# Kernel tuning notes

Hardware: AMD Instinct MI355X
Metric: run time of the kernel (lower is better)

Reference implementation:

```python
import jax, jax.numpy as jnp
import numpy as np

NUM_HEADS = 8
D_MODEL = 512
D_K = D_MODEL // NUM_HEADS


def setup_inputs() -> dict:
    key = jax.random.key(0)
    ks = jax.random.split(key, 8)
    B, C, L = 4, D_MODEL, 2048
    s = 1.0 / np.sqrt(C)  # xavier-ish scale for 1x1 convs
    return {
        "X_q": jax.random.normal(ks[0], (B, C, L), jnp.float32),
        "X_k": jax.random.normal(ks[1], (B, C, L), jnp.float32),
        "X_v": jax.random.normal(ks[2], (B, C, L), jnp.float32),
        "Wq": jax.random.normal(ks[3], (D_MODEL, C), jnp.float32) * s,
        "Wk": jax.random.normal(ks[4], (D_MODEL, C), jnp.float32) * s,
        "Wv": jax.random.normal(ks[5], (D_MODEL, C), jnp.float32) * s,
        "Wh": jax.random.normal(ks[6], (D_MODEL, D_MODEL), jnp.float32) * s,
        "bh": jnp.zeros((D_MODEL,), jnp.float32),
    }


def reference(X_q, X_k, X_v, Wq, Wk, Wv, Wh, bh):
    B, C, L = X_q.shape
    H, dk = NUM_HEADS, D_K

    def proj(x, W):  # 1x1 Conv1d, no bias: (B,Cin,L) -> (B,Cout,L)
        return jnp.einsum("oc,bcl->bol", W, x)

    # split_heads: (B, d_model, L) -> (B, H, d_k, L)
    Q = proj(X_q, Wq).reshape(B, H, dk, L)
    K = proj(X_k, Wk).reshape(B, H, dk, L)
    V = proj(X_v, Wv).reshape(B, H, dk, L)

    Q = Q / np.sqrt(dk).astype(np.float32)
    # scores: Q^T K -> (B, H, L_q, L_k)
    scores = jnp.einsum("bhdq,bhdk->bhqk", Q, K)
    A = jax.nn.softmax(scores, axis=-1)
    # H = A @ V^T -> (B, H, L, d_k); dropout is identity at eval
    Hh = jnp.einsum("bhqk,bhdk->bhqd", A, V)
    # group_heads: (B,H,L,dk) -> (B,H,dk,L) -> (B, d_model, L)
    H_cat = Hh.transpose(0, 1, 3, 2).reshape(B, H * dk, L)
    out = jnp.einsum("oc,bcl->bol", Wh, H_cat) + bh[None, :, None]
    return (out, A)
```

## Files before the change

### kernel.cpp

```cpp
#include <hip/hip_runtime.h>

#define L_SEQ 2048
#define CDIM  512
#define NB    4
#define NH    8
#define DKH   64

typedef __attribute__((ext_vector_type(8))) __bf16 bf16x8;
typedef __attribute__((ext_vector_type(4))) float  f32x4;
typedef __attribute__((ext_vector_type(8))) unsigned short u16x8;

__device__ __forceinline__ unsigned short f2bf(float f) {
  union { float f; unsigned u; } x; x.f = f;
  unsigned r = x.u + 0x7FFFu + ((x.u >> 16) & 1u);
  return (unsigned short)(r >> 16);
}
__device__ __forceinline__ float bf2f(unsigned short u) {
  union { unsigned u; float f; } x; x.u = ((unsigned)u) << 16;
  return x.f;
}
__device__ __forceinline__ bf16x8 ldfrag(const unsigned short* p) {
  u16x8 v = *reinterpret_cast<const u16x8*>(p);
  return __builtin_bit_cast(bf16x8, v);
}
#define MFMA(a,b,c) __builtin_amdgcn_mfma_f32_16x16x32_bf16((a),(b),(c),0,0,0)

__global__ __launch_bounds__(256) void k_cast(const float* __restrict__ X,
                                              unsigned short* __restrict__ Y, int n) {
  int i = (blockIdx.x * 256 + threadIdx.x) * 8;
  if (i + 8 > n) return;
  const float4* p = reinterpret_cast<const float4*>(X + i);
  float4 a = p[0], b = p[1];
  u16x8 o;
  o[0]=f2bf(a.x); o[1]=f2bf(a.y); o[2]=f2bf(a.z); o[3]=f2bf(a.w);
  o[4]=f2bf(b.x); o[5]=f2bf(b.y); o[6]=f2bf(b.z); o[7]=f2bf(b.w);
  *reinterpret_cast<u16x8*>(Y + i) = o;
}

__global__ __launch_bounds__(256) void k_transpose(const float* __restrict__ X,
                                                   unsigned short* __restrict__ Xt) {
  __shared__ __align__(16) unsigned short t[64][72];
  int l0 = blockIdx.x * 64, c0 = blockIdx.y * 64;
  size_t boff = (size_t)blockIdx.z * CDIM * L_SEQ;
  const float* Xb = X + boff;
  unsigned short* Xtb = Xt + boff;
  int tid = threadIdx.x;
  int cc = tid >> 2, lo = (tid & 3) * 16;
  const float* src = Xb + (size_t)(c0 + cc) * L_SEQ + l0 + lo;
#pragma unroll
  for (int i = 0; i < 4; ++i) {
    float4 v = *reinterpret_cast<const float4*>(src + i * 4);
    t[lo + i*4 + 0][cc] = f2bf(v.x);
    t[lo + i*4 + 1][cc] = f2bf(v.y);
    t[lo + i*4 + 2][cc] = f2bf(v.z);
    t[lo + i*4 + 3][cc] = f2bf(v.w);
  }
  __syncthreads();
  int ll = tid >> 2, co = (tid & 3) * 16;
  unsigned short* dst = Xtb + (size_t)(l0 + ll) * CDIM + c0 + co;
  u16x8 a = *reinterpret_cast<const u16x8*>(&t[ll][co]);
  u16x8 b = *reinterpret_cast<const u16x8*>(&t[ll][co + 8]);
  *reinterpret_cast<u16x8*>(dst) = a;
  *reinterpret_cast<u16x8*>(dst + 8) = b;
}

template<int OUT_BF16, int HAS_BIAS>
__global__ __launch_bounds__(256) void k_gemm_nt(
    const unsigned short* __restrict__ A, long sA,
    const unsigned short* __restrict__ Bt, long sB,
    void* __restrict__ Out, long sO,
    const float* __restrict__ bias, float scale, int M, int N) {
  __shared__ __align__(16) unsigned short lA[128 * 64];
  __shared__ __align__(16) unsigned short lB[128 * 64];
  int b = blockIdx.z;
  const unsigned short* Ab = A + (size_t)b * sA;
  const unsigned short* Bb = Bt + (size_t)b * sB;
  int m0 = blockIdx.y * 128, n0 = blockIdx.x * 128;
  int tid = threadIdx.x, lane = tid & 63, wave = tid >> 6;
  int wm = (wave >> 1) * 64, wn = (wave & 1) * 64;
  f32x4 acc[4][4] = {};
  int srow = tid >> 3;
  int sslot = tid & 7;

  for (int k0 = 0; k0 < 512; k0 += 64) {
    __syncthreads();
#pragma unroll
    for (int i = 0; i < 4; ++i) {
      int r = srow + 32 * i;
      int sw = (sslot ^ (r & 7)) * 8;
      u16x8 va = *reinterpret_cast<const u16x8*>(Ab + (size_t)(m0 + r) * 512 + k0 + sslot * 8);
      *reinterpret_cast<u16x8*>(&lA[r * 64 + sw]) = va;
      u16x8 vb = *reinterpret_cast<const u16x8*>(Bb + (size_t)(n0 + r) * 512 + k0 + sslot * 8);
      *reinterpret_cast<u16x8*>(&lB[r * 64 + sw]) = vb;
    }
    __syncthreads();
#pragma unroll
    for (int c = 0; c < 2; ++c) {
      bf16x8 af[4], bfr[4];
#pragma unroll
      for (int t = 0; t < 4; ++t) {
        int ra = wm + t * 16 + (lane & 15);
        int sa = (lane >> 4) + 4 * c;
        af[t] = ldfrag(&lA[ra * 64 + ((sa ^ (ra & 7)) * 8)]);
        int rb = wn + t * 16 + (lane & 15);
        bfr[t] = ldfrag(&lB[rb * 64 + ((sa ^ (rb & 7)) * 8)]);
      }
#pragma unroll
      for (int i = 0; i < 4; ++i)
#pragma unroll
        for (int j = 0; j < 4; ++j)
          acc[i][j] = MFMA(af[i], bfr[j], acc[i][j]);
    }
  }
  int row4 = (lane >> 4) * 4, col = lane & 15;
#pragma unroll
  for (int i = 0; i < 4; ++i)
#pragma unroll
    for (int j = 0; j < 4; ++j)
#pragma unroll
      for (int e = 0; e < 4; ++e) {
        int r = m0 + wm + i * 16 + row4 + e;
        int cN = n0 + wn + j * 16 + col;
        float v = acc[i][j][e] * scale;
        if (HAS_BIAS) v += bias[r];
        size_t idx = (size_t)b * sO + (size_t)r * N + cN;
        if (OUT_BF16) ((unsigned short*)Out)[idx] = f2bf(v);
        else          ((float*)Out)[idx] = v;
      }
}

__global__ __launch_bounds__(256) void k_attn(
    const unsigned short* __restrict__ Qt,
    const unsigned short* __restrict__ Kt,
    const unsigned short* __restrict__ Vn,
    unsigned short* __restrict__ HhT,
    float* __restrict__ Aout) {
  __shared__ __align__(16) unsigned short a_lds[4][1024];
  int bh = blockIdx.y;
  int b = bh >> 3, h = bh & 7;
  int lane = threadIdx.x & 63, wave = threadIdx.x >> 6;
  int q0 = blockIdx.x * 64 + wave * 16;
  const unsigned short* Qh = Qt + (size_t)b * L_SEQ * CDIM + h * DKH;
  const unsigned short* Kh = Kt + (size_t)b * L_SEQ * CDIM + h * DKH;
  const unsigned short* Vh = Vn + (size_t)b * CDIM * L_SEQ + (size_t)h * DKH * L_SEQ;
  unsigned short* Ho = HhT + (size_t)b * L_SEQ * CDIM + h * DKH;
  float* Ab = Aout + (size_t)bh * L_SEQ * L_SEQ;

  int fr = lane & 15, fg = lane >> 4;
  bf16x8 qf0 = ldfrag(Qh + (size_t)(q0 + fr) * CDIM + fg * 8);
  bf16x8 qf1 = ldfrag(Qh + (size_t)(q0 + fr) * CDIM + fg * 8 + 32);

  float psum[4] = {0.f, 0.f, 0.f, 0.f};
  for (int kt = 0; kt < L_SEQ; kt += 64) {
#pragma unroll
    for (int t = 0; t < 4; ++t) {
      const unsigned short* kp = Kh + (size_t)(kt + t * 16 + fr) * CDIM + fg * 8;
      f32x4 s = {0.f, 0.f, 0.f, 0.f};
      s = MFMA(qf0, ldfrag(kp), s);
      s = MFMA(qf1, ldfrag(kp + 32), s);
#pragma unroll
      for (int e = 0; e < 4; ++e) psum[e] += __expf(s[e]);
    }
  }
#pragma unroll
  for (int e = 0; e < 4; ++e) {
    psum[e] += __shfl_xor(psum[e], 1, 64);
    psum[e] += __shfl_xor(psum[e], 2, 64);
    psum[e] += __shfl_xor(psum[e], 4, 64);
    psum[e] += __shfl_xor(psum[e], 8, 64);
  }
  float inv[4];
#pragma unroll
  for (int e = 0; e < 4; ++e) inv[e] = 1.0f / psum[e];

  f32x4 oacc[4] = {};
  unsigned short* al = a_lds[wave];
  for (int kt = 0; kt < L_SEQ; kt += 64) {
    f32x4 sv[4];
#pragma unroll
    for (int t = 0; t < 4; ++t) {
      const unsigned short* kp = Kh + (size_t)(kt + t * 16 + fr) * CDIM + fg * 8;
      f32x4 s = {0.f, 0.f, 0.f, 0.f};
      s = MFMA(qf0, ldfrag(kp), s);
      s = MFMA(qf1, ldfrag(kp + 32), s);
      sv[t] = s;
    }
#pragma unroll
    for (int t = 0; t < 4; ++t)
#pragma unroll
      for (int e = 0; e < 4; ++e) {
        float a = __expf(sv[t][e]) * inv[e];
        int row = fg * 4 + e;
        int byte = ((row * 128 + (t * 16 + fr) * 2)) ^ ((row & 7) << 4);
        al[byte >> 1] = f2bf(a);
      }
    {
      int wrow = lane >> 2;
      int slot0 = (lane & 3) * 2;
      int by0 = ((wrow * 128 + slot0 * 16)) ^ ((wrow & 7) << 4);
      int by1 = ((wrow * 128 + (slot0 + 1) * 16)) ^ ((wrow & 7) << 4);
      u16x8 p0 = *reinterpret_cast<const u16x8*>(al + (by0 >> 1));
      u16x8 p1 = *reinterpret_cast<const u16x8*>(al + (by1 >> 1));
      float* dp = Ab + (size_t)(q0 + wrow) * L_SEQ + kt + (lane & 3) * 16;
      float4 f0 = {bf2f(p0[0]), bf2f(p0[1]), bf2f(p0[2]), bf2f(p0[3])};
      float4 f1 = {bf2f(p0[4]), bf2f(p0[5]), bf2f(p0[6]), bf2f(p0[7])};
      float4 f2 = {bf2f(p1[0]), bf2f(p1[1]), bf2f(p1[2]), bf2f(p1[3])};
      float4 f3 = {bf2f(p1[4]), bf2f(p1[5]), bf2f(p1[6]), bf2f(p1[7])};
      *reinterpret_cast<float4*>(dp + 0)  = f0;
      *reinterpret_cast<float4*>(dp + 4)  = f1;
      *reinterpret_cast<float4*>(dp + 8)  = f2;
      *reinterpret_cast<float4*>(dp + 12) = f3;
    }
    int byA0 = ((fr * 128 + fg * 16)) ^ ((fr & 7) << 4);
    int byA1 = ((fr * 128 + (fg + 4) * 16)) ^ ((fr & 7) << 4);
    bf16x8 af0 = ldfrag(al + (byA0 >> 1));
    bf16x8 af1 = ldfrag(al + (byA1 >> 1));
#pragma unroll
    for (int nt = 0; nt < 4; ++nt) {
      const unsigned short* vp = Vh + (size_t)(nt * 16 + fr) * L_SEQ + kt + fg * 8;
      oacc[nt] = MFMA(af0, ldfrag(vp), oacc[nt]);
      oacc[nt] = MFMA(af1, ldfrag(vp + 32), oacc[nt]);
    }
  }
#pragma unroll
  for (int nt = 0; nt < 4; ++nt)
#pragma unroll
    for (int e = 0; e < 4; ++e)
      Ho[(size_t)(q0 + fg * 4 + e) * CDIM + nt * 16 + fr] = f2bf(oacc[nt][e]);
}

extern "C" void kernel_launch(void* const* d_in, const int* in_sizes, int n_in,
                              void* d_out, int out_size, void* d_ws, size_t ws_size,
                              hipStream_t stream) {
  const float* Xq = (const float*)d_in[0];
  const float* Xk = (const float*)d_in[1];
  const float* Xv = (const float*)d_in[2];
  const float* Wq = (const float*)d_in[3];
  const float* Wk = (const float*)d_in[4];
  const float* Wv = (const float*)d_in[5];
  const float* Wh = (const float*)d_in[6];
  const float* bh = (const float*)d_in[7];

  const size_t PROJ = (size_t)NB * L_SEQ * CDIM;
  float* out_f = (float*)d_out;
  float* A_out = out_f + PROJ;

  unsigned short* Qt = (unsigned short*)d_out;
  unsigned short* Kt = Qt + PROJ;
  unsigned short* Xtq = (unsigned short*)A_out;
  unsigned short* Xtk = Xtq + PROJ;
  unsigned short* Xtv = Xtk + PROJ;
  unsigned short* Vn  = (unsigned short*)d_ws;
  unsigned short* HhT = Vn + PROJ;
  unsigned short* Wqb = HhT + PROJ;
  unsigned short* Wkb = Wqb + CDIM * CDIM;
  unsigned short* Wvb = Wkb + CDIM * CDIM;
  unsigned short* Whb = Wvb + CDIM * CDIM;

  int nW = CDIM * CDIM;
  k_cast<<<nW / 2048, 256, 0, stream>>>(Wq, Wqb, nW);
  k_cast<<<nW / 2048, 256, 0, stream>>>(Wk, Wkb, nW);
  k_cast<<<nW / 2048, 256, 0, stream>>>(Wv, Wvb, nW);
  k_cast<<<nW / 2048, 256, 0, stream>>>(Wh, Whb, nW);

  dim3 tg(L_SEQ / 64, CDIM / 64, NB);
  k_transpose<<<tg, 256, 0, stream>>>(Xq, Xtq);
  k_transpose<<<tg, 256, 0, stream>>>(Xk, Xtk);
  k_transpose<<<tg, 256, 0, stream>>>(Xv, Xtv);

  const long sLC = (long)L_SEQ * CDIM;
  k_gemm_nt<1, 0><<<dim3(CDIM / 128, L_SEQ / 128, NB), 256, 0, stream>>>(
      Xtq, sLC, Wqb, 0, Qt, sLC, nullptr, 0.125f, L_SEQ, CDIM);
  k_gemm_nt<1, 0><<<dim3(CDIM / 128, L_SEQ / 128, NB), 256, 0, stream>>>(
      Xtk, sLC, Wkb, 0, Kt, sLC, nullptr, 1.0f, L_SEQ, CDIM);
  k_gemm_nt<1, 0><<<dim3(L_SEQ / 128, CDIM / 128, NB), 256, 0, stream>>>(
      Wvb, 0, Xtv, sLC, Vn, sLC, nullptr, 1.0f, CDIM, L_SEQ);

  k_attn<<<dim3(L_SEQ / 64, NB * NH), 256, 0, stream>>>(Qt, Kt, Vn, HhT, A_out);

  k_gemm_nt<0, 1><<<dim3(L_SEQ / 128, CDIM / 128, NB), 256, 0, stream>>>(
      Whb, 0, HhT, sLC, out_f, sLC, bh, 1.0f, CDIM, L_SEQ);
}
```

Baseline: 540.6 us.

## Stage K/V tiles in LDS via async global_load_lds double buffering; use exp2

The attention kernel now loads K and V tiles cooperatively into double-buffered, XOR-swizzled LDS using global_load_lds. Each wave previously read the same K and V from global memory on its own, and the async loads are meant to overlap the next tile's fetch with compute. The softmax exponent now uses the raw v_exp_f32 (exp2) instruction, with log2(e) folded into the Q projection scale. The A matrix stores become nontemporal to avoid cache pollution. In exchange it adds a block-wide barrier on every tile and uses more LDS per block, which may lower occupancy.

After: 824.2 us. 52.5% more time.

```diff
diff --git a/kernel.cpp b/kernel.cpp
--- a/kernel.cpp
+++ b/kernel.cpp
@@ -23,7 +23,14 @@
   u16x8 v = *reinterpret_cast<const u16x8*>(p);
   return __builtin_bit_cast(bf16x8, v);
 }
+__device__ __forceinline__ float fexp2(float x) {
+  float r; asm("v_exp_f32 %0, %1" : "=v"(r) : "v"(x)); return r;
+}
 #define MFMA(a,b,c) __builtin_amdgcn_mfma_f32_16x16x32_bf16((a),(b),(c),0,0,0)
+
+#define GLOADLDS(gp, lp) __builtin_amdgcn_global_load_lds( \
+    (const __attribute__((address_space(1))) void*)(gp),   \
+    (__attribute__((address_space(3))) void*)(lp), 16, 0, 0)
 
 __global__ __launch_bounds__(256) void k_cast(const float* __restrict__ X,
                                               unsigned short* __restrict__ Y, int n) {
@@ -135,10 +142,13 @@
     const unsigned short* __restrict__ Vn,
     unsigned short* __restrict__ HhT,
     float* __restrict__ Aout) {
-  __shared__ __align__(16) unsigned short a_lds[4][1024];
+  __shared__ __align__(16) unsigned short Kb[2][4096];
+  __shared__ __align__(16) unsigned short Vb[2][4096];
+  __shared__ __align__(16) unsigned short al[4][1024];
   int bh = blockIdx.y;
   int b = bh >> 3, h = bh & 7;
-  int lane = threadIdx.x & 63, wave = threadIdx.x >> 6;
+  int tid = threadIdx.x;
+  int lane = tid & 63, wave = tid >> 6;
   int q0 = blockIdx.x * 64 + wave * 16;
   const unsigned short* Qh = Qt + (size_t)b * L_SEQ * CDIM + h * DKH;
   const unsigned short* Kh = Kt + (size_t)b * L_SEQ * CDIM + h * DKH;
@@ -150,17 +160,41 @@
   bf16x8 qf0 = ldfrag(Qh + (size_t)(q0 + fr) * CDIM + fg * 8);
   bf16x8 qf1 = ldfrag(Qh + (size_t)(q0 + fr) * CDIM + fg * 8 + 32);
 
+  int rowin = lane >> 3;
+  int slot = (lane & 7) ^ rowin;
+  int c0 = wave * 2, c1 = wave * 2 + 1;
+  const unsigned short* gk0 = Kh + (size_t)(c0 * 8 + rowin) * CDIM + slot * 8;
+  const unsigned short* gk1 = Kh + (size_t)(c1 * 8 + rowin) * CDIM + slot * 8;
+  const unsigned short* gv0 = Vh + (size_t)(c0 * 8 + rowin) * L_SEQ + slot * 8;
+  const unsigned short* gv1 = Vh + (size_t)(c1 * 8 + rowin) * L_SEQ + slot * 8;
+
+#define STAGE_K(bi, ktoff) do { \
+    GLOADLDS(gk0 + (size_t)(ktoff) * CDIM, &Kb[bi][c0 * 512]); \
+    GLOADLDS(gk1 + (size_t)(ktoff) * CDIM, &Kb[bi][c1 * 512]); } while (0)
+#define STAGE_V(bi, ktoff) do { \
+    GLOADLDS(gv0 + (ktoff), &Vb[bi][c0 * 512]); \
+    GLOADLDS(gv1 + (ktoff), &Vb[bi][c1 * 512]); } while (0)
+
   float psum[4] = {0.f, 0.f, 0.f, 0.f};
-  for (int kt = 0; kt < L_SEQ; kt += 64) {
+  STAGE_K(0, 0);
+  __syncthreads();
+  int buf = 0;
+  for (int i = 0; i < 32; ++i) {
+    if (i < 31) STAGE_K(buf ^ 1, (i + 1) * 64);
+    const unsigned short* kb = Kb[buf];
 #pragma unroll
     for (int t = 0; t < 4; ++t) {
-      const unsigned short* kp = Kh + (size_t)(kt + t * 16 + fr) * CDIM + fg * 8;
+      int r = t * 16 + fr;
+      bf16x8 kf0 = ldfrag(kb + r * 64 + ((fg ^ (r & 7)) * 8));
+      bf16x8 kf1 = ldfrag(kb + r * 64 + (((fg + 4) ^ (r & 7)) * 8));
       f32x4 s = {0.f, 0.f, 0.f, 0.f};
-      s = MFMA(qf0, ldfrag(kp), s);
-      s = MFMA(qf1, ldfrag(kp + 32), s);
-#pragma unroll
-      for (int e = 0; e < 4; ++e) psum[e] += __expf(s[e]);
-    }
+      s = MFMA(qf0, kf0, s);
+      s = MFMA(qf1, kf1, s);
+#pragma unroll
+      for (int e = 0; e < 4; ++e) psum[e] += fexp2(s[e]);
+    }
+    __syncthreads();
+    buf ^= 1;
   }
 #pragma unroll
   for (int e = 0; e < 4; ++e) {
@@ -174,59 +208,75 @@
   for (int e = 0; e < 4; ++e) inv[e] = 1.0f / psum[e];
 
   f32x4 oacc[4] = {};
-  unsigned short* al = a_lds[wave];
-  for (int kt = 0; kt < L_SEQ; kt += 64) {
+  unsigned short* alw = al[wave];
+  STAGE_K(0, 0);
+  STAGE_V(0, 0);
+  __syncthreads();
+  buf = 0;
+  for (int i = 0; i < 32; ++i) {
+    int kt = i * 64;
+    if (i < 31) { STAGE_K(buf ^ 1, kt + 64); STAGE_V(buf ^ 1, kt + 64); }
+    const unsigned short* kb = Kb[buf];
+    const unsigned short* vb = Vb[buf];
     f32x4 sv[4];
 #pragma unroll
     for (int t = 0; t < 4; ++t) {
-      const unsigned short* kp = Kh + (size_t)(kt + t * 16 + fr) * CDIM + fg * 8;
+      int r = t * 16 + fr;
+      bf16x8 kf0 = ldfrag(kb + r * 64 + ((fg ^ (r & 7)) * 8));
+      bf16x8 kf1 = ldfrag(kb + r * 64 + (((fg + 4) ^ (r & 7)) * 8));
       f32x4 s = {0.f, 0.f, 0.f, 0.f};
-      s = MFMA(qf0, ldfrag(kp), s);
-      s = MFMA(qf1, ldfrag(kp + 32), s);
+      s = MFMA(qf0, kf0, s);
+      s = MFMA(qf1, kf1, s);
       sv[t] = s;
     }
 #pragma unroll
     for (int t = 0; t < 4; ++t)
 #pragma unroll
       for (int e = 0; e < 4; ++e) {
-        float a = __expf(sv[t][e]) * inv[e];
+        float a = fexp2(sv[t][e]) * inv[e];
         int row = fg * 4 + e;
-        int byte = ((row * 128 + (t * 16 + fr) * 2)) ^ ((row & 7) << 4);
-        al[byte >> 1] = f2bf(a);
+        int byte = (row * 128 + (t * 16 + fr) * 2) ^ ((row & 7) << 4);
+        alw[byte >> 1] = f2bf(a);
       }
     {
       int wrow = lane >> 2;
       int slot0 = (lane & 3) * 2;
-      int by0 = ((wrow * 128 + slot0 * 16)) ^ ((wrow & 7) << 4);
-      int by1 = ((wrow * 128 + (slot0 + 1) * 16)) ^ ((wrow & 7) << 4);
-      u16x8 p0 = *reinterpret_cast<const u16x8*>(al + (by0 >> 1));
-      u16x8 p1 = *reinterpret_cast<const u16x8*>(al + (by1 >> 1));
+      int by0 = (wrow * 128 + slot0 * 16) ^ ((wrow & 7) << 4);
+      int by1 = (wrow * 128 + (slot0 + 1) * 16) ^ ((wrow & 7) << 4);
+      u16x8 p0 = *reinterpret_cast<const u16x8*>(alw + (by0 >> 1));
+      u16x8 p1 = *reinterpret_cast<const u16x8*>(alw + (by1 >> 1));
       float* dp = Ab + (size_t)(q0 + wrow) * L_SEQ + kt + (lane & 3) * 16;
-      float4 f0 = {bf2f(p0[0]), bf2f(p0[1]), bf2f(p0[2]), bf2f(p0[3])};
-      float4 f1 = {bf2f(p0[4]), bf2f(p0[5]), bf2f(p0[6]), bf2f(p0[7])};
-      float4 f2 = {bf2f(p1[0]), bf2f(p1[1]), bf2f(p1[2]), bf2f(p1[3])};
-      float4 f3 = {bf2f(p1[4]), bf2f(p1[5]), bf2f(p1[6]), bf2f(p1[7])};
-      *reinterpret_cast<float4*>(dp + 0)  = f0;
-      *reinterpret_cast<float4*>(dp + 4)  = f1;
-      *reinterpret_cast<float4*>(dp + 8)  = f2;
-      *reinterpret_cast<float4*>(dp + 12) = f3;
-    }
-    int byA0 = ((fr * 128 + fg * 16)) ^ ((fr & 7) << 4);
-    int byA1 = ((fr * 128 + (fg + 4) * 16)) ^ ((fr & 7) << 4);
-    bf16x8 af0 = ldfrag(al + (byA0 >> 1));
-    bf16x8 af1 = ldfrag(al + (byA1 >> 1));
+      f32x4 f0 = {bf2f(p0[0]), bf2f(p0[1]), bf2f(p0[2]), bf2f(p0[3])};
+      f32x4 f1 = {bf2f(p0[4]), bf2f(p0[5]), bf2f(p0[6]), bf2f(p0[7])};
+      f32x4 f2 = {bf2f(p1[0]), bf2f(p1[1]), bf2f(p1[2]), bf2f(p1[3])};
+      f32x4 f3 = {bf2f(p1[4]), bf2f(p1[5]), bf2f(p1[6]), bf2f(p1[7])};
+      __builtin_nontemporal_store(f0, reinterpret_cast<f32x4*>(dp + 0));
+      __builtin_nontemporal_store(f1, reinterpret_cast<f32x4*>(dp + 4));
+      __builtin_nontemporal_store(f2, reinterpret_cast<f32x4*>(dp + 8));
+      __builtin_nontemporal_store(f3, reinterpret_cast<f32x4*>(dp + 12));
+    }
+    int byA0 = (fr * 128 + fg * 16) ^ ((fr & 7) << 4);
+    int byA1 = (fr * 128 + (fg + 4) * 16) ^ ((fr & 7) << 4);
+    bf16x8 af0 = ldfrag(alw + (byA0 >> 1));
+    bf16x8 af1 = ldfrag(alw + (byA1 >> 1));
 #pragma unroll
     for (int nt = 0; nt < 4; ++nt) {
-      const unsigned short* vp = Vh + (size_t)(nt * 16 + fr) * L_SEQ + kt + fg * 8;
-      oacc[nt] = MFMA(af0, ldfrag(vp), oacc[nt]);
-      oacc[nt] = MFMA(af1, ldfrag(vp + 32), oacc[nt]);
-    }
+      int r = nt * 16 + fr;
+      bf16x8 vf0 = ldfrag(vb + r * 64 + ((fg ^ (r & 7)) * 8));
+      bf16x8 vf1 = ldfrag(vb + r * 64 + (((fg + 4) ^ (r & 7)) * 8));
+      oacc[nt] = MFMA(af0, vf0, oacc[nt]);
+      oacc[nt] = MFMA(af1, vf1, oacc[nt]);
+    }
+    __syncthreads();
+    buf ^= 1;
   }
 #pragma unroll
   for (int nt = 0; nt < 4; ++nt)
 #pragma unroll
     for (int e = 0; e < 4; ++e)
       Ho[(size_t)(q0 + fg * 4 + e) * CDIM + nt * 16 + fr] = f2bf(oacc[nt][e]);
+#undef STAGE_K
+#undef STAGE_V
 }
 
 extern "C" void kernel_launch(void* const* d_in, const int* in_sizes, int n_in,
@@ -270,7 +320,7 @@
 
   const long sLC = (long)L_SEQ * CDIM;
   k_gemm_nt<1, 0><<<dim3(CDIM / 128, L_SEQ / 128, NB), 256, 0, stream>>>(
-      Xtq, sLC, Wqb, 0, Qt, sLC, nullptr, 0.125f, L_SEQ, CDIM);
+      Xtq, sLC, Wqb, 0, Qt, sLC, nullptr, 0.18033688f, L_SEQ, CDIM);
   k_gemm_nt<1, 0><<<dim3(CDIM / 128, L_SEQ / 128, NB), 256, 0, stream>>>(
       Xtk, sLC, Wkb, 0, Kt, sLC, nullptr, 1.0f, L_SEQ, CDIM);
   k_gemm_nt<1, 0><<<dim3(L_SEQ / 128, CDIM / 128, NB), 256, 0, stream>>>(
```

## Double-buffer K loads in attention and fold log2e into Q scale for exp2

Applied to the files above, without the earlier changes.

The attention kernel now prefetches the next 64-key tile of K fragments into registers (ping-pong buffers) while computing on the current one, and issues V loads ahead of the softmax work. The Q projection scale now includes log2(e), so the kernel can use the raw v_exp_f32 (exp2) instruction instead of __expf. This aims to hide global-load latency and shave ALU work in the exp, at the cost of higher register pressure. The loadset(vr, vbase, 0, 0) call is redundant work that gets overwritten.

Result: faster. 519.8 us (-3.8%).

```diff
diff --git a/kernel.cpp b/kernel.cpp
--- a/kernel.cpp
+++ b/kernel.cpp
@@ -23,7 +23,21 @@
   u16x8 v = *reinterpret_cast<const u16x8*>(p);
   return __builtin_bit_cast(bf16x8, v);
 }
+__device__ __forceinline__ bf16x8 asbf(u16x8 v) { return __builtin_bit_cast(bf16x8, v); }
+__device__ __forceinline__ float fexp2(float x) {
+  float r; asm("v_exp_f32 %0, %1" : "=v"(r) : "v"(x)); return r;
+}
 #define MFMA(a,b,c) __builtin_amdgcn_mfma_f32_16x16x32_bf16((a),(b),(c),0,0,0)
+
+__device__ __forceinline__ void loadset(u16x8* dst, const unsigned short* base,
+                                        int kt, long stride) {
+#pragma unroll
+  for (int t = 0; t < 4; ++t) {
+    const unsigned short* p = base + (size_t)(kt + t * 16) * stride;
+    dst[2*t]   = *reinterpret_cast<const u16x8*>(p);
+    dst[2*t+1] = *reinterpret_cast<const u16x8*>(p + 32);
+  }
+}
 
 __global__ __launch_bounds__(256) void k_cast(const float* __restrict__ X,
                                               unsigned short* __restrict__ Y, int n) {
@@ -135,7 +149,7 @@
     const unsigned short* __restrict__ Vn,
     unsigned short* __restrict__ HhT,
     float* __restrict__ Aout) {
-  __shared__ __align__(16) unsigned short a_lds[4][1024];
+  __shared__ __align__(16) unsigned short al[4][1024];
   int bh = blockIdx.y;
   int b = bh >> 3, h = bh & 7;
   int lane = threadIdx.x & 63, wave = threadIdx.x >> 6;
@@ -150,16 +164,28 @@
   bf16x8 qf0 = ldfrag(Qh + (size_t)(q0 + fr) * CDIM + fg * 8);
   bf16x8 qf1 = ldfrag(Qh + (size_t)(q0 + fr) * CDIM + fg * 8 + 32);
 
+  const unsigned short* kbase = Kh + (size_t)fr * CDIM + fg * 8;
+  const unsigned short* vbase = Vh + (size_t)fr * L_SEQ + fg * 8;
+
   float psum[4] = {0.f, 0.f, 0.f, 0.f};
-  for (int kt = 0; kt < L_SEQ; kt += 64) {
-#pragma unroll
-    for (int t = 0; t < 4; ++t) {
-      const unsigned short* kp = Kh + (size_t)(kt + t * 16 + fr) * CDIM + fg * 8;
-      f32x4 s = {0.f, 0.f, 0.f, 0.f};
-      s = MFMA(qf0, ldfrag(kp), s);
-      s = MFMA(qf1, ldfrag(kp + 32), s);
-#pragma unroll
-      for (int e = 0; e < 4; ++e) psum[e] += __expf(s[e]);
+  {
+    u16x8 ka[8], kb2[8];
+    auto half1 = [&](const u16x8* ks) {
+#pragma unroll
+      for (int t = 0; t < 4; ++t) {
+        f32x4 s = {0.f, 0.f, 0.f, 0.f};
+        s = MFMA(qf0, asbf(ks[2*t]), s);
+        s = MFMA(qf1, asbf(ks[2*t+1]), s);
+#pragma unroll
+        for (int e = 0; e < 4; ++e) psum[e] += fexp2(s[e]);
+      }
+    };
+    loadset(ka, kbase, 0, CDIM);
+    for (int i = 0; i < 32; i += 2) {
+      loadset(kb2, kbase, (i + 1) * 64, CDIM);
+      half1(ka);
+      loadset(ka, kbase, ((i + 2) & 31) * 64, CDIM);
+      half1(kb2);
     }
   }
 #pragma unroll
@@ -174,52 +200,64 @@
   for (int e = 0; e < 4; ++e) inv[e] = 1.0f / psum[e];
 
   f32x4 oacc[4] = {};
-  unsigned short* al = a_lds[wave];
-  for (int kt = 0; kt < L_SEQ; kt += 64) {
-    f32x4 sv[4];
-#pragma unroll
-    for (int t = 0; t < 4; ++t) {
-      const unsigned short* kp = Kh + (size_t)(kt + t * 16 + fr) * CDIM + fg * 8;
-      f32x4 s = {0.f, 0.f, 0.f, 0.f};
-      s = MFMA(qf0, ldfrag(kp), s);
-      s = MFMA(qf1, ldfrag(kp + 32), s);
-      sv[t] = s;
-    }
-#pragma unroll
-    for (int t = 0; t < 4; ++t)
-#pragma unroll
-      for (int e = 0; e < 4; ++e) {
-        float a = __expf(sv[t][e]) * inv[e];
-        int row = fg * 4 + e;
-        int byte = ((row * 128 + (t * 16 + fr) * 2)) ^ ((row & 7) << 4);
-        al[byte >> 1] = f2bf(a);
-      }
-    {
-      int wrow = lane >> 2;
-      int slot0 = (lane & 3) * 2;
-      int by0 = ((wrow * 128 + slot0 * 16)) ^ ((wrow & 7) << 4);
-      int by1 = ((wrow * 128 + (slot0 + 1) * 16)) ^ ((wrow & 7) << 4);
-      u16x8 p0 = *reinterpret_cast<const u16x8*>(al + (by0 >> 1));
-      u16x8 p1 = *reinterpret_cast<const u16x8*>(al + (by1 >> 1));
-      float* dp = Ab + (size_t)(q0 + wrow) * L_SEQ + kt + (lane & 3) * 16;
-      float4 f0 = {bf2f(p0[0]), bf2f(p0[1]), bf2f(p0[2]), bf2f(p0[3])};
-      float4 f1 = {bf2f(p0[4]), bf2f(p0[5]), bf2f(p0[6]), bf2f(p0[7])};
-      float4 f2 = {bf2f(p1[0]), bf2f(p1[1]), bf2f(p1[2]), bf2f(p1[3])};
-      float4 f3 = {bf2f(p1[4]), bf2f(p1[5]), bf2f(p1[6]), bf2f(p1[7])};
-      *reinterpret_cast<float4*>(dp + 0)  = f0;
-      *reinterpret_cast<float4*>(dp + 4)  = f1;
-      *reinterpret_cast<float4*>(dp + 8)  = f2;
-      *reinterpret_cast<float4*>(dp + 12) = f3;
-    }
-    int byA0 = ((fr * 128 + fg * 16)) ^ ((fr & 7) << 4);
-    int byA1 = ((fr * 128 + (fg + 4) * 16)) ^ ((fr & 7) << 4);
-    bf16x8 af0 = ldfrag(al + (byA0 >> 1));
-    bf16x8 af1 = ldfrag(al + (byA1 >> 1));
-#pragma unroll
-    for (int nt = 0; nt < 4; ++nt) {
-      const unsigned short* vp = Vh + (size_t)(nt * 16 + fr) * L_SEQ + kt + fg * 8;
-      oacc[nt] = MFMA(af0, ldfrag(vp), oacc[nt]);
-      oacc[nt] = MFMA(af1, ldfrag(vp + 32), oacc[nt]);
+  unsigned short* alw = al[wave];
+  {
+    u16x8 ka[8], kb2[8];
+    auto half2 = [&](const u16x8* ks, int kt) {
+      u16x8 vr[8];
+      loadset(vr, vbase, 0, 0);
+#pragma unroll
+      for (int nt = 0; nt < 4; ++nt) {
+        const unsigned short* vp = vbase + (size_t)(nt * 16) * L_SEQ + kt;
+        vr[2*nt]   = *reinterpret_cast<const u16x8*>(vp);
+        vr[2*nt+1] = *reinterpret_cast<const u16x8*>(vp + 32);
+      }
+#pragma unroll
+      for (int t = 0; t < 4; ++t) {
+        f32x4 s = {0.f, 0.f, 0.f, 0.f};
+        s = MFMA(qf0, asbf(ks[2*t]), s);
+        s = MFMA(qf1, asbf(ks[2*t+1]), s);
+#pragma unroll
+        for (int e = 0; e < 4; ++e) {
+          float a = fexp2(s[e]) * inv[e];
+          int row = fg * 4 + e;
+          int byte = (row * 128 + (t * 16 + fr) * 2) ^ ((row & 7) << 4);
+          alw[byte >> 1] = f2bf(a);
+        }
+      }
+      {
+        int wrow = lane >> 2;
+        int slot0 = (lane & 3) * 2;
+        int by0 = (wrow * 128 + slot0 * 16) ^ ((wrow & 7) << 4);
+        int by1 = (wrow * 128 + (slot0 + 1) * 16) ^ ((wrow & 7) << 4);
+        u16x8 p0 = *reinterpret_cast<const u16x8*>(alw + (by0 >> 1));
+        u16x8 p1 = *reinterpret_cast<const u16x8*>(alw + (by1 >> 1));
+        float* dp = Ab + (size_t)(q0 + wrow) * L_SEQ + kt + (lane & 3) * 16;
+        f32x4 f0 = {bf2f(p0[0]), bf2f(p0[1]), bf2f(p0[2]), bf2f(p0[3])};
+        f32x4 f1 = {bf2f(p0[4]), bf2f(p0[5]), bf2f(p0[6]), bf2f(p0[7])};
+        f32x4 f2 = {bf2f(p1[0]), bf2f(p1[1]), bf2f(p1[2]), bf2f(p1[3])};
+        f32x4 f3 = {bf2f(p1[4]), bf2f(p1[5]), bf2f(p1[6]), bf2f(p1[7])};
+        *reinterpret_cast<f32x4*>(dp + 0)  = f0;
+        *reinterpret_cast<f32x4*>(dp + 4)  = f1;
+        *reinterpret_cast<f32x4*>(dp + 8)  = f2;
+        *reinterpret_cast<f32x4*>(dp + 12) = f3;
+      }
+      int byA0 = (fr * 128 + fg * 16) ^ ((fr & 7) << 4);
+      int byA1 = (fr * 128 + (fg + 4) * 16) ^ ((fr & 7) << 4);
+      bf16x8 af0 = ldfrag(alw + (byA0 >> 1));
+      bf16x8 af1 = ldfrag(alw + (byA1 >> 1));
+#pragma unroll
+      for (int nt = 0; nt < 4; ++nt) {
+        oacc[nt] = MFMA(af0, asbf(vr[2*nt]), oacc[nt]);
+        oacc[nt] = MFMA(af1, asbf(vr[2*nt+1]), oacc[nt]);
+      }
+    };
+    loadset(ka, kbase, 0, CDIM);
+    for (int i = 0; i < 32; i += 2) {
+      loadset(kb2, kbase, (i + 1) * 64, CDIM);
+      half2(ka, i * 64);
+      loadset(ka, kbase, ((i + 2) & 31) * 64, CDIM);
+      half2(kb2, (i + 1) * 64);
     }
   }
 #pragma unroll
@@ -270,7 +308,7 @@
 
   const long sLC = (long)L_SEQ * CDIM;
   k_gemm_nt<1, 0><<<dim3(CDIM / 128, L_SEQ / 128, NB), 256, 0, stream>>>(
-      Xtq, sLC, Wqb, 0, Qt, sLC, nullptr, 0.125f, L_SEQ, CDIM);
+      Xtq, sLC, Wqb, 0, Qt, sLC, nullptr, 0.18033688f, L_SEQ, CDIM);
   k_gemm_nt<1, 0><<<dim3(CDIM / 128, L_SEQ / 128, NB), 256, 0, stream>>>(
       Xtk, sLC, Wkb, 0, Kt, sLC, nullptr, 1.0f, L_SEQ, CDIM);
   k_gemm_nt<1, 0><<<dim3(L_SEQ / 128, CDIM / 128, NB), 256, 0, stream>>>(
```
